# Kernel tuning notes

Measured on AMD Instinct MI355X. Metric: run time of the kernel, lower is better.

The kernel has to match this reference:

```python
import jax, jax.numpy as jnp
import numpy as np

LEAKY_ALPHA = 0.2  # TF default for tf.nn.leaky_relu

def setup_inputs() -> dict:
    key = jax.random.key(0)
    k1, k2, k3 = jax.random.split(key, 3)
    B, N, D = 8192, 2048, 128
    patient_features = jax.random.normal(k1, (B, D), dtype=jnp.float32)
    disease_nodes = jax.random.normal(k2, (N, D), dtype=jnp.float32)
    attn_kernel = jax.random.normal(k3, (2 * D, 1), dtype=jnp.float32)
    return {"patient_features": patient_features,
            "disease_nodes": disease_nodes,
            "attn_kernel": attn_kernel}

def reference(patient_features, disease_nodes, attn_kernel):
    # patient_features: [B, D]; disease_nodes: [N, D]; attn_kernel: [2D, 1]
    D = patient_features.shape[-1]
    a_p = attn_kernel[:D, 0]   # [D] acts on the patient half of the concat
    a_n = attn_kernel[D:, 0]   # [D] acts on the disease-node half
    # concat([p, n]) @ a  ==  p @ a_p  +  n @ a_n  (exact decomposition)
    scores = (patient_features @ a_p)[:, None] + (disease_nodes @ a_n)[None, :]  # [B, N]
    attn_weights = jax.nn.softmax(jax.nn.leaky_relu(scores, LEAKY_ALPHA), axis=1)  # [B, N]
    node_influence = attn_weights @ disease_nodes  # [B, D]
    return patient_features + node_influence
```

## Files before the change

kernel.cpp:

```cpp
#include <hip/hip_runtime.h>
#include <hip/hip_bf16.h>

#define LEAKY 0.2f
#define B_TOT 8192
#define N_TOT 2048
#define D_TOT 128
#define BM 16

typedef float f32x4 __attribute__((ext_vector_type(4)));
typedef short bf16x8 __attribute__((ext_vector_type(8)));
typedef unsigned short u16x8 __attribute__((ext_vector_type(8)));

static __device__ __forceinline__ unsigned short f2bf(float x) {
    return __builtin_bit_cast(unsigned short, __float2bfloat16(x));
}


__global__ __launch_bounds__(256) void prep_kernel(const float* __restrict__ disease,
                                                   const float* __restrict__ ak,
                                                   float* __restrict__ q,
                                                   uint4* __restrict__ DnTf) {
    __shared__ float tile[32][129];
    __shared__ float a_s[D_TOT];
    const int tid = threadIdx.x;
    const int b = blockIdx.x;
    const int r0 = b * 32;

    if (tid < D_TOT) a_s[tid] = ak[D_TOT + tid];
    #pragma unroll
    for (int t = 0; t < 4; ++t) {
        int idx = tid + t * 256;
        int row = idx >> 5;
        int cv = (idx & 31) * 4;
        float4 v = *(const float4*)(disease + (size_t)(r0 + row) * D_TOT + cv);
        tile[row][cv] = v.x; tile[row][cv + 1] = v.y;
        tile[row][cv + 2] = v.z; tile[row][cv + 3] = v.w;
    }
    __syncthreads();

    const int wave = tid >> 6, lane = tid & 63;
    #pragma unroll
    for (int rr = 0; rr < 8; ++rr) {
        int r = wave * 8 + rr;
        float s = tile[r][lane] * a_s[lane] + tile[r][lane + 64] * a_s[lane + 64];
        #pragma unroll
        for (int off = 32; off; off >>= 1) s += __shfl_xor(s, off);
        if (lane == 0) q[r0 + r] = s;
    }

    #pragma unroll
    for (int h = 0; h < 2; ++h) {
        const int c  = tid + h * 256;
        const int kg = c >> 7;
        const int col = c & 127;
        const int ct = col >> 4, cl = col & 15;
        unsigned u[4];
        #pragma unroll
        for (int jj = 0; jj < 4; ++jj) {
            unsigned lo = f2bf(tile[kg * 8 + 2 * jj][col]);
            unsigned hi = f2bf(tile[kg * 8 + 2 * jj + 1][col]);
            u[jj] = lo | (hi << 16);
        }
        DnTf[((size_t)b * 8 + ct) * 64 + kg * 16 + cl] = make_uint4(u[0], u[1], u[2], u[3]);
    }
}

__global__ __launch_bounds__(1024, 8) void gat_mfma(const float* __restrict__ patient,
                                                    const float* __restrict__ ak,
                                                    const float* __restrict__ q,
                                                    const unsigned short* __restrict__ DnTb,
                                                    float* __restrict__ out) {
    __shared__ __align__(16) float eq1_s[N_TOT];
    __shared__ __align__(16) float eq2_s[N_TOT];
    __shared__ float red_s[7][2][1024];
    __shared__ float a_s[D_TOT];
    __shared__ float p_s[BM], E1_s[BM], E2_s[BM], S_s[BM];
    __shared__ float red16[16];

    const int tid  = threadIdx.x;
    const int wave = tid >> 6;
    const int lane = tid & 63;
    const int b0   = blockIdx.x * BM;

    if (tid < D_TOT) a_s[tid] = ak[tid];
    __syncthreads();

    float mx = -1e30f;
    for (int i = tid; i < N_TOT; i += 1024) {
        float qq = q[i];
        eq1_s[i] = __expf(qq);
        eq2_s[i] = __expf(LEAKY * qq);
        mx = fmaxf(mx, qq);
    }
    #pragma unroll
    for (int off = 32; off; off >>= 1) mx = fmaxf(mx, __shfl_xor(mx, off));
    if (lane == 0) red16[wave] = mx;

    {
        const float* pr = patient + (size_t)(b0 + wave) * D_TOT;
        float s = pr[lane] * a_s[lane] + pr[lane + 64] * a_s[lane + 64];
        #pragma unroll
        for (int off = 32; off; off >>= 1) s += __shfl_xor(s, off);
        if (lane == 0) p_s[wave] = s;
    }
    __syncthreads();

    if (tid < BM) {
        float qmax = red16[0];
        #pragma unroll
        for (int i = 1; i < 16; ++i) qmax = fmaxf(qmax, red16[i]);
        const float pv = p_s[tid];
        const float xm = pv + qmax;
        const float m = fmaxf(xm, LEAKY * xm);
        E1_s[tid] = __expf(pv - m);
        E2_s[tid] = __expf(LEAKY * pv - m);
    }
    __syncthreads();

    {
        const float E1 = E1_s[wave], E2 = E2_s[wave];
        float s = 0.f;
        for (int n = lane; n < N_TOT; n += 64)
            s += fmaxf(E1 * eq1_s[n], E2 * eq2_s[n]);
        #pragma unroll
        for (int off = 32; off; off >>= 1) s += __shfl_xor(s, off);
        if (lane == 0) S_s[wave] = s;
    }
    __syncthreads();

    const int cl = lane & 15;
    const int kg = lane >> 4;
    const int cw = wave & 1;
    const int kq = wave >> 1;

    const float E1A = E1_s[cl], E2A = E2_s[cl];

    f32x4 acc[4] = {};

    #pragma unroll 2
    for (int kt = kq * 8; kt < kq * 8 + 8; ++kt) {
        const int gk = kt * 32 + kg * 8;
        const float4 e1a = *(const float4*)&eq1_s[gk];
        const float4 e1b = *(const float4*)&eq1_s[gk + 4];
        const float4 e2a = *(const float4*)&eq2_s[gk];
        const float4 e2b = *(const float4*)&eq2_s[gk + 4];
        bf16x8 bf[4];
        #pragma unroll
        for (int t = 0; t < 4; ++t)
            bf[t] = *(const bf16x8*)(DnTb + (((size_t)kt * 8 + cw * 4 + t) * 64 + lane) * 8);

        const float e1v[8] = {e1a.x, e1a.y, e1a.z, e1a.w, e1b.x, e1b.y, e1b.z, e1b.w};
        const float e2v[8] = {e2a.x, e2a.y, e2a.z, e2a.w, e2b.x, e2b.y, e2b.z, e2b.w};
        u16x8 aw;
        #pragma unroll
        for (int j = 0; j < 8; ++j)
            aw[j] = f2bf(fmaxf(E1A * e1v[j], E2A * e2v[j]));
        const bf16x8 a0 = __builtin_bit_cast(bf16x8, aw);

        acc[0] = __builtin_amdgcn_mfma_f32_16x16x32_bf16(a0, bf[0], acc[0], 0, 0, 0);
        acc[1] = __builtin_amdgcn_mfma_f32_16x16x32_bf16(a0, bf[1], acc[1], 0, 0, 0);
        acc[2] = __builtin_amdgcn_mfma_f32_16x16x32_bf16(a0, bf[2], acc[2], 0, 0, 0);
        acc[3] = __builtin_amdgcn_mfma_f32_16x16x32_bf16(a0, bf[3], acc[3], 0, 0, 0);
    }

    __syncthreads();
    if (kq > 0) {
        float* rb = &red_s[kq - 1][cw][0];
        #pragma unroll
        for (int t = 0; t < 4; ++t)
            #pragma unroll
            for (int i = 0; i < 4; ++i)
                rb[t * 256 + (kg * 4 + i) * 16 + cl] = acc[t][i];
    }
    __syncthreads();
    if (kq == 0) {
        #pragma unroll
        for (int t = 0; t < 4; ++t)
            #pragma unroll
            for (int i = 0; i < 4; ++i) {
                const int idx = t * 256 + (kg * 4 + i) * 16 + cl;
                float s = acc[t][i];
                #pragma unroll
                for (int j = 0; j < 7; ++j) s += red_s[j][cw][idx];
                acc[t][i] = s;
            }
        float inv[4];
        #pragma unroll
        for (int i = 0; i < 4; ++i) inv[i] = 1.0f / S_s[kg * 4 + i];
        #pragma unroll
        for (int t = 0; t < 4; ++t)
            #pragma unroll
            for (int i = 0; i < 4; ++i) {
                const int row = b0 + kg * 4 + i;
                const int col = cw * 64 + t * 16 + cl;
                out[(size_t)row * D_TOT + col] =
                    patient[(size_t)row * D_TOT + col] + acc[t][i] * inv[i];
            }
    }
}


__global__ __launch_bounds__(256) void pq_fb(const float* __restrict__ patient,
                                             const float* __restrict__ disease,
                                             const float* __restrict__ ak,
                                             float* __restrict__ p,
                                             float* __restrict__ q) {
    int gid  = blockIdx.x * blockDim.x + threadIdx.x;
    int wid  = gid >> 6;
    int lane = gid & 63;
    const float* src;
    const float* a;
    float* dst;
    if (wid < B_TOT) {
        src = patient + (size_t)wid * D_TOT; a = ak; dst = p + wid;
    } else {
        src = disease + (size_t)(wid - B_TOT) * D_TOT; a = ak + D_TOT; dst = q + (wid - B_TOT);
    }
    float s = src[lane] * a[lane] + src[lane + 64] * a[lane + 64];
    #pragma unroll
    for (int off = 32; off; off >>= 1) s += __shfl_xor(s, off);
    if (lane == 0) *dst = s;
}

#define FBP 16
#define FNT 256
__global__ __launch_bounds__(256) void gat_fb(const float* __restrict__ patient,
                                              const float* __restrict__ disease,
                                              const float* __restrict__ p,
                                              const float* __restrict__ q,
                                              float* __restrict__ out) {
    __shared__ float q_s[N_TOT];
    __shared__ float w_s[FBP][FNT];
    __shared__ float m_s[FBP], S_s[FBP], pp_s[FBP];
    const int tid = threadIdx.x;
    const int b0  = blockIdx.x * FBP;
    for (int i = tid; i < N_TOT; i += 256) q_s[i] = q[i];
    if (tid < FBP) pp_s[tid] = p[b0 + tid];
    __syncthreads();
    const int wave = tid >> 6, lane = tid & 63;
    for (int pi = wave * 4; pi < wave * 4 + 4; ++pi) {
        float pp = pp_s[pi];
        float mx = -1e30f;
        for (int n = lane; n < N_TOT; n += 64) {
            float x = pp + q_s[n]; x = x > 0.0f ? x : LEAKY * x; mx = fmaxf(mx, x);
        }
        #pragma unroll
        for (int off = 32; off; off >>= 1) mx = fmaxf(mx, __shfl_xor(mx, off));
        float sum = 0.0f;
        for (int n = lane; n < N_TOT; n += 64) {
            float x = pp + q_s[n]; x = x > 0.0f ? x : LEAKY * x; sum += __expf(x - mx);
        }
        #pragma unroll
        for (int off = 32; off; off >>= 1) sum += __shfl_xor(sum, off);
        if (lane == 0) { m_s[pi] = mx; S_s[pi] = sum; }
    }
    __syncthreads();
    const int d2 = tid & 31;
    const int pg = tid >> 5;
    const int p0 = 2 * pg, p1 = 2 * pg + 1;
    float4 acc0 = make_float4(0.f, 0.f, 0.f, 0.f);
    float4 acc1 = make_float4(0.f, 0.f, 0.f, 0.f);
    for (int n0 = 0; n0 < N_TOT; n0 += FNT) {
        __syncthreads();
        for (int i = tid; i < FBP * FNT; i += 256) {
            int pi = i >> 8;
            int nt = i & (FNT - 1);
            float x = pp_s[pi] + q_s[n0 + nt];
            x = x > 0.0f ? x : LEAKY * x;
            w_s[pi][nt] = __expf(x - m_s[pi]);
        }
        __syncthreads();
        const float* drow = disease + (size_t)n0 * D_TOT + d2 * 4;
        #pragma unroll 4
        for (int nt = 0; nt < FNT; ++nt) {
            float4 dv = *reinterpret_cast<const float4*>(drow + (size_t)nt * D_TOT);
            float w0 = w_s[p0][nt];
            float w1 = w_s[p1][nt];
            acc0.x += w0 * dv.x; acc0.y += w0 * dv.y; acc0.z += w0 * dv.z; acc0.w += w0 * dv.w;
            acc1.x += w1 * dv.x; acc1.y += w1 * dv.y; acc1.z += w1 * dv.z; acc1.w += w1 * dv.w;
        }
    }
    const float inv0 = 1.0f / S_s[p0];
    const float inv1 = 1.0f / S_s[p1];
    {
        size_t off = (size_t)(b0 + p0) * D_TOT + d2 * 4;
        float4 pf = *reinterpret_cast<const float4*>(patient + off);
        float4 o;
        o.x = pf.x + acc0.x * inv0; o.y = pf.y + acc0.y * inv0;
        o.z = pf.z + acc0.z * inv0; o.w = pf.w + acc0.w * inv0;
        *reinterpret_cast<float4*>(reinterpret_cast<float*>(out) + off) = o;
    }
    {
        size_t off = (size_t)(b0 + p1) * D_TOT + d2 * 4;
        float4 pf = *reinterpret_cast<const float4*>(patient + off);
        float4 o;
        o.x = pf.x + acc1.x * inv1; o.y = pf.y + acc1.y * inv1;
        o.z = pf.z + acc1.z * inv1; o.w = pf.w + acc1.w * inv1;
        *reinterpret_cast<float4*>(reinterpret_cast<float*>(out) + off) = o;
    }
}

extern "C" void kernel_launch(void* const* d_in, const int* in_sizes, int n_in,
                              void* d_out, int out_size, void* d_ws, size_t ws_size,
                              hipStream_t stream) {
    const float* patient = (const float*)d_in[0];
    const float* disease = (const float*)d_in[1];
    const float* ak      = (const float*)d_in[2];
    float* out = (float*)d_out;

    const size_t need_fast = (size_t)512 * 1024 + 8192;
    if (ws_size >= need_fast) {
        uint4* DnTf = (uint4*)d_ws;
        float* q    = (float*)((char*)d_ws + 512 * 1024);
        prep_kernel<<<N_TOT / 32, 256, 0, stream>>>(disease, ak, q, DnTf);
        gat_mfma<<<B_TOT / BM, 1024, 0, stream>>>(patient, ak, q,
                                                  (const unsigned short*)DnTf, out);
    } else {
        float* p = (float*)d_ws;
        float* q = p + B_TOT;
        pq_fb<<<(B_TOT + N_TOT) / 4, 256, 0, stream>>>(patient, disease, ak, p, q);
        gat_fb<<<B_TOT / FBP, 256, 0, stream>>>(patient, disease, p, q, out);
    }
}
```

Before: 29.07 us.

## Replace dense attention GEMM with sorted-threshold prefix-sum formulation

The scores are rank-1 (p_b + q_n), so the leaky-relu branch depends only on whether q_n > -p_b. The new path sorts q by rank counting and builds per-column prefix and suffix sums of exp(q)·disease and exp(0.2q)·disease. Each patient row then needs only a binary search and a few O(D) lookups instead of a full N×D product. This removes the B×N×D MFMA work but adds three small serial kernels (rank, scan, pq). It also brings fp32 cancellation risk from subtracting prefix sums, and needs a larger workspace.

New measurement: 39.78 us. +36.8%, slower.

```diff
diff --git a/kernel.cpp b/kernel.cpp
--- a/kernel.cpp
+++ b/kernel.cpp
@@ -5,7 +5,6 @@
 #define B_TOT 8192
 #define N_TOT 2048
 #define D_TOT 128
-#define BM 16
 
 typedef float f32x4 __attribute__((ext_vector_type(4)));
 typedef short bf16x8 __attribute__((ext_vector_type(8)));
@@ -14,191 +13,6 @@
 static __device__ __forceinline__ unsigned short f2bf(float x) {
     return __builtin_bit_cast(unsigned short, __float2bfloat16(x));
 }
-
-
-__global__ __launch_bounds__(256) void prep_kernel(const float* __restrict__ disease,
-                                                   const float* __restrict__ ak,
-                                                   float* __restrict__ q,
-                                                   uint4* __restrict__ DnTf) {
-    __shared__ float tile[32][129];
-    __shared__ float a_s[D_TOT];
-    const int tid = threadIdx.x;
-    const int b = blockIdx.x;
-    const int r0 = b * 32;
-
-    if (tid < D_TOT) a_s[tid] = ak[D_TOT + tid];
-    #pragma unroll
-    for (int t = 0; t < 4; ++t) {
-        int idx = tid + t * 256;
-        int row = idx >> 5;
-        int cv = (idx & 31) * 4;
-        float4 v = *(const float4*)(disease + (size_t)(r0 + row) * D_TOT + cv);
-        tile[row][cv] = v.x; tile[row][cv + 1] = v.y;
-        tile[row][cv + 2] = v.z; tile[row][cv + 3] = v.w;
-    }
-    __syncthreads();
-
-    const int wave = tid >> 6, lane = tid & 63;
-    #pragma unroll
-    for (int rr = 0; rr < 8; ++rr) {
-        int r = wave * 8 + rr;
-        float s = tile[r][lane] * a_s[lane] + tile[r][lane + 64] * a_s[lane + 64];
-        #pragma unroll
-        for (int off = 32; off; off >>= 1) s += __shfl_xor(s, off);
-        if (lane == 0) q[r0 + r] = s;
-    }
-
-    #pragma unroll
-    for (int h = 0; h < 2; ++h) {
-        const int c  = tid + h * 256;
-        const int kg = c >> 7;
-        const int col = c & 127;
-        const int ct = col >> 4, cl = col & 15;
-        unsigned u[4];
-        #pragma unroll
-        for (int jj = 0; jj < 4; ++jj) {
-            unsigned lo = f2bf(tile[kg * 8 + 2 * jj][col]);
-            unsigned hi = f2bf(tile[kg * 8 + 2 * jj + 1][col]);
-            u[jj] = lo | (hi << 16);
-        }
-        DnTf[((size_t)b * 8 + ct) * 64 + kg * 16 + cl] = make_uint4(u[0], u[1], u[2], u[3]);
-    }
-}
-
-__global__ __launch_bounds__(1024, 8) void gat_mfma(const float* __restrict__ patient,
-                                                    const float* __restrict__ ak,
-                                                    const float* __restrict__ q,
-                                                    const unsigned short* __restrict__ DnTb,
-                                                    float* __restrict__ out) {
-    __shared__ __align__(16) float eq1_s[N_TOT];
-    __shared__ __align__(16) float eq2_s[N_TOT];
-    __shared__ float red_s[7][2][1024];
-    __shared__ float a_s[D_TOT];
-    __shared__ float p_s[BM], E1_s[BM], E2_s[BM], S_s[BM];
-    __shared__ float red16[16];
-
-    const int tid  = threadIdx.x;
-    const int wave = tid >> 6;
-    const int lane = tid & 63;
-    const int b0   = blockIdx.x * BM;
-
-    if (tid < D_TOT) a_s[tid] = ak[tid];
-    __syncthreads();
-
-    float mx = -1e30f;
-    for (int i = tid; i < N_TOT; i += 1024) {
-        float qq = q[i];
-        eq1_s[i] = __expf(qq);
-        eq2_s[i] = __expf(LEAKY * qq);
-        mx = fmaxf(mx, qq);
-    }
-    #pragma unroll
-    for (int off = 32; off; off >>= 1) mx = fmaxf(mx, __shfl_xor(mx, off));
-    if (lane == 0) red16[wave] = mx;
-
-    {
-        const float* pr = patient + (size_t)(b0 + wave) * D_TOT;
-        float s = pr[lane] * a_s[lane] + pr[lane + 64] * a_s[lane + 64];
-        #pragma unroll
-        for (int off = 32; off; off >>= 1) s += __shfl_xor(s, off);
-        if (lane == 0) p_s[wave] = s;
-    }
-    __syncthreads();
-
-    if (tid < BM) {
-        float qmax = red16[0];
-        #pragma unroll
-        for (int i = 1; i < 16; ++i) qmax = fmaxf(qmax, red16[i]);
-        const float pv = p_s[tid];
-        const float xm = pv + qmax;
-        const float m = fmaxf(xm, LEAKY * xm);
-        E1_s[tid] = __expf(pv - m);
-        E2_s[tid] = __expf(LEAKY * pv - m);
-    }
-    __syncthreads();
-
-    {
-        const float E1 = E1_s[wave], E2 = E2_s[wave];
-        float s = 0.f;
-        for (int n = lane; n < N_TOT; n += 64)
-            s += fmaxf(E1 * eq1_s[n], E2 * eq2_s[n]);
-        #pragma unroll
-        for (int off = 32; off; off >>= 1) s += __shfl_xor(s, off);
-        if (lane == 0) S_s[wave] = s;
-    }
-    __syncthreads();
-
-    const int cl = lane & 15;
-    const int kg = lane >> 4;
-    const int cw = wave & 1;
-    const int kq = wave >> 1;
-
-    const float E1A = E1_s[cl], E2A = E2_s[cl];
-
-    f32x4 acc[4] = {};
-
-    #pragma unroll 2
-    for (int kt = kq * 8; kt < kq * 8 + 8; ++kt) {
-        const int gk = kt * 32 + kg * 8;
-        const float4 e1a = *(const float4*)&eq1_s[gk];
-        const float4 e1b = *(const float4*)&eq1_s[gk + 4];
-        const float4 e2a = *(const float4*)&eq2_s[gk];
-        const float4 e2b = *(const float4*)&eq2_s[gk + 4];
-        bf16x8 bf[4];
-        #pragma unroll
-        for (int t = 0; t < 4; ++t)
-            bf[t] = *(const bf16x8*)(DnTb + (((size_t)kt * 8 + cw * 4 + t) * 64 + lane) * 8);
-
-        const float e1v[8] = {e1a.x, e1a.y, e1a.z, e1a.w, e1b.x, e1b.y, e1b.z, e1b.w};
-        const float e2v[8] = {e2a.x, e2a.y, e2a.z, e2a.w, e2b.x, e2b.y, e2b.z, e2b.w};
-        u16x8 aw;
-        #pragma unroll
-        for (int j = 0; j < 8; ++j)
-            aw[j] = f2bf(fmaxf(E1A * e1v[j], E2A * e2v[j]));
-        const bf16x8 a0 = __builtin_bit_cast(bf16x8, aw);
-
-        acc[0] = __builtin_amdgcn_mfma_f32_16x16x32_bf16(a0, bf[0], acc[0], 0, 0, 0);
-        acc[1] = __builtin_amdgcn_mfma_f32_16x16x32_bf16(a0, bf[1], acc[1], 0, 0, 0);
-        acc[2] = __builtin_amdgcn_mfma_f32_16x16x32_bf16(a0, bf[2], acc[2], 0, 0, 0);
-        acc[3] = __builtin_amdgcn_mfma_f32_16x16x32_bf16(a0, bf[3], acc[3], 0, 0, 0);
-    }
-
-    __syncthreads();
-    if (kq > 0) {
-        float* rb = &red_s[kq - 1][cw][0];
-        #pragma unroll
-        for (int t = 0; t < 4; ++t)
-            #pragma unroll
-            for (int i = 0; i < 4; ++i)
-                rb[t * 256 + (kg * 4 + i) * 16 + cl] = acc[t][i];
-    }
-    __syncthreads();
-    if (kq == 0) {
-        #pragma unroll
-        for (int t = 0; t < 4; ++t)
-            #pragma unroll
-            for (int i = 0; i < 4; ++i) {
-                const int idx = t * 256 + (kg * 4 + i) * 16 + cl;
-                float s = acc[t][i];
-                #pragma unroll
-                for (int j = 0; j < 7; ++j) s += red_s[j][cw][idx];
-                acc[t][i] = s;
-            }
-        float inv[4];
-        #pragma unroll
-        for (int i = 0; i < 4; ++i) inv[i] = 1.0f / S_s[kg * 4 + i];
-        #pragma unroll
-        for (int t = 0; t < 4; ++t)
-            #pragma unroll
-            for (int i = 0; i < 4; ++i) {
-                const int row = b0 + kg * 4 + i;
-                const int col = cw * 64 + t * 16 + cl;
-                out[(size_t)row * D_TOT + col] =
-                    patient[(size_t)row * D_TOT + col] + acc[t][i] * inv[i];
-            }
-    }
-}
-
 
 __global__ __launch_bounds__(256) void pq_fb(const float* __restrict__ patient,
                                              const float* __restrict__ disease,
@@ -222,6 +36,357 @@
     if (lane == 0) *dst = s;
 }
 
+__global__ __launch_bounds__(256) void rank_kernel(const float* __restrict__ q,
+                                                   float* __restrict__ sortedq,
+                                                   float* __restrict__ eq1s,
+                                                   float* __restrict__ eq2s,
+                                                   int* __restrict__ perm) {
+    __shared__ float q_s[N_TOT];
+    const int tid = threadIdx.x;
+    for (int i = tid; i < N_TOT; i += 256) q_s[i] = q[i];
+    __syncthreads();
+    const int kl = tid >> 2, sub = tid & 3;
+    const int k = blockIdx.x * 64 + kl;
+    const float qk = q_s[k];
+    int cnt = 0;
+    const int j0 = sub * 512;
+    for (int j = j0; j < j0 + 512; ++j) {
+        float qj = q_s[j];
+        cnt += (qj < qk || (qj == qk && j < k)) ? 1 : 0;
+    }
+    cnt += __shfl_xor(cnt, 1);
+    cnt += __shfl_xor(cnt, 2);
+    if (sub == 0) {
+        sortedq[cnt] = qk;
+        perm[cnt]    = k;
+        eq1s[cnt]    = __expf(qk);
+        eq2s[cnt]    = __expf(LEAKY * qk);
+    }
+}
+
+__global__ __launch_bounds__(256) void scan_kernel(const float* __restrict__ disease,
+                                                   const float* __restrict__ eq1s,
+                                                   const float* __restrict__ eq2s,
+                                                   const int* __restrict__ perm,
+                                                   float* __restrict__ P1,
+                                                   float* __restrict__ P2,
+                                                   float* __restrict__ T1,
+                                                   float* __restrict__ T2,
+                                                   float* __restrict__ S1suf,
+                                                   float* __restrict__ S2pre) {
+    const int tid = threadIdx.x;
+    const int b = blockIdx.x;
+    if (b < 32) {
+        __shared__ int   perm_s[64];
+        __shared__ float e1l[64], e2l[64];
+        const int r0 = b * 64;
+        if (tid < 64) {
+            perm_s[tid] = perm[r0 + tid];
+            e1l[tid] = eq1s[r0 + tid];
+            e2l[tid] = eq2s[r0 + tid];
+        }
+        __syncthreads();
+        const int table = tid >> 7, col = tid & 127;
+        float run = 0.f;
+        float* Pt = table ? P2 : P1;
+        #pragma unroll 4
+        for (int j = 0; j < 64; ++j) {
+            const float d = disease[(size_t)perm_s[j] * D_TOT + col];
+            const float v = (table ? e2l[j] : e1l[j]) * d;
+            Pt[(size_t)(r0 + j) * D_TOT + col] = run;
+            run += v;
+        }
+        (table ? T2 : T1)[b * 128 + col] = run;
+    } else {
+        __shared__ float v_s[N_TOT];
+        __shared__ float wtot[4];
+        __shared__ float tot_s;
+        const int lane = tid & 63, wv = tid >> 6;
+        for (int pass = 0; pass < 2; ++pass) {
+            const float* src = pass == 0 ? eq1s : eq2s;
+            for (int i = tid; i < N_TOT; i += 256) v_s[i] = src[i];
+            __syncthreads();
+            float s[8];
+            float run = 0.f;
+            #pragma unroll
+            for (int i = 0; i < 8; ++i) { run += v_s[tid * 8 + i]; s[i] = run; }
+            float incl = run;
+            #pragma unroll
+            for (int off = 1; off < 64; off <<= 1) {
+                float v = __shfl_up(incl, off);
+                if (lane >= off) incl += v;
+            }
+            if (lane == 63) wtot[wv] = incl;
+            __syncthreads();
+            float woff = 0.f;
+            for (int w = 0; w < wv; ++w) woff += wtot[w];
+            const float base = woff + incl - run;
+            if (tid == 255) tot_s = woff + incl;
+            __syncthreads();
+            const float tot = tot_s;
+            if (pass == 0) {
+                #pragma unroll
+                for (int i = 0; i < 8; ++i) {
+                    float EP = base + (i ? s[i - 1] : 0.f);
+                    S1suf[tid * 8 + i] = tot - EP;
+                }
+                if (tid == 255) S1suf[N_TOT] = 0.f;
+            } else {
+                #pragma unroll
+                for (int i = 0; i < 8; ++i)
+                    S2pre[tid * 8 + i] = base + (i ? s[i - 1] : 0.f);
+                if (tid == 255) S2pre[N_TOT] = tot;
+            }
+            __syncthreads();
+        }
+    }
+}
+
+__global__ __launch_bounds__(256) void gat_ps(const float* __restrict__ patient,
+                                              const float* __restrict__ p,
+                                              const float* __restrict__ sortedq,
+                                              const float* __restrict__ P1,
+                                              const float* __restrict__ P2,
+                                              const float* __restrict__ T1,
+                                              const float* __restrict__ T2,
+                                              const float* __restrict__ S1suf,
+                                              const float* __restrict__ S2pre,
+                                              float* __restrict__ out) {
+    __shared__ float sq[N_TOT];
+    __shared__ float suf1[33][128];
+    __shared__ float pre2[33][128];
+    __shared__ float e1_s[32], e2_s[32], inv_s[32];
+    __shared__ int   c_s[32];
+    const int tid = threadIdx.x;
+    const int b0 = blockIdx.x * 32;
+
+    for (int i = tid; i < N_TOT; i += 256) sq[i] = sortedq[i];
+
+    if (tid < 128) {
+        float r = 0.f;
+        suf1[32][tid] = 0.f;
+        for (int b = 31; b >= 0; --b) { r += T1[b * 128 + tid]; suf1[b][tid] = r; }
+    } else {
+        const int col = tid - 128;
+        float r = 0.f;
+        for (int b = 0; b < 32; ++b) { pre2[b][col] = r; r += T2[b * 128 + col]; }
+        pre2[32][col] = r;
+    }
+    __syncthreads();
+
+    if (tid < 32) {
+        const float pv = p[b0 + tid];
+        const float qmax = sq[N_TOT - 1];
+        const float xm = pv + qmax;
+        const float m = fmaxf(xm, LEAKY * xm);
+        const float E1 = __expf(pv - m);
+        const float E2 = __expf(LEAKY * pv - m);
+        const float thr = -pv;
+        int lo = 0, hi = N_TOT;
+        while (lo < hi) {
+            int mid = (lo + hi) >> 1;
+            if (sq[mid] <= thr) lo = mid + 1; else hi = mid;
+        }
+        const float S = E1 * S1suf[lo] + E2 * S2pre[lo];
+        e1_s[tid] = E1; e2_s[tid] = E2; inv_s[tid] = 1.0f / S; c_s[tid] = lo;
+    }
+    __syncthreads();
+
+    const int row = tid >> 3;
+    const int cb = (tid & 7) * 16;
+    const int gr = b0 + row;
+    const int c = c_s[row];
+    const int bc = c >> 6;
+    const float E1 = e1_s[row], E2 = e2_s[row], inv = inv_s[row];
+    const bool has = (c < N_TOT);
+
+    #pragma unroll
+    for (int i = 0; i < 4; ++i) {
+        const int col = cb + i * 4;
+        float4 p1 = make_float4(0.f, 0.f, 0.f, 0.f);
+        float4 p2 = make_float4(0.f, 0.f, 0.f, 0.f);
+        if (has) {
+            p1 = *(const float4*)&P1[(size_t)c * D_TOT + col];
+            p2 = *(const float4*)&P2[(size_t)c * D_TOT + col];
+        }
+        const float4 pat = *(const float4*)&patient[(size_t)gr * D_TOT + col];
+        float4 o;
+        o.x = pat.x + (E1 * (suf1[bc][col + 0] - p1.x) + E2 * (pre2[bc][col + 0] + p2.x)) * inv;
+        o.y = pat.y + (E1 * (suf1[bc][col + 1] - p1.y) + E2 * (pre2[bc][col + 1] + p2.y)) * inv;
+        o.z = pat.z + (E1 * (suf1[bc][col + 2] - p1.z) + E2 * (pre2[bc][col + 2] + p2.z)) * inv;
+        o.w = pat.w + (E1 * (suf1[bc][col + 3] - p1.w) + E2 * (pre2[bc][col + 3] + p2.w)) * inv;
+        *(float4*)&out[(size_t)gr * D_TOT + col] = o;
+    }
+}
+
+#define MBM 16
+__global__ __launch_bounds__(256) void prep_kernel(const float* __restrict__ disease,
+                                                   const float* __restrict__ ak,
+                                                   float* __restrict__ q,
+                                                   uint4* __restrict__ DnTf) {
+    __shared__ float tile[32][129];
+    __shared__ float a_s[D_TOT];
+    const int tid = threadIdx.x;
+    const int b = blockIdx.x;
+    const int r0 = b * 32;
+    if (tid < D_TOT) a_s[tid] = ak[D_TOT + tid];
+    #pragma unroll
+    for (int t = 0; t < 4; ++t) {
+        int idx = tid + t * 256;
+        int row = idx >> 5;
+        int cv = (idx & 31) * 4;
+        float4 v = *(const float4*)(disease + (size_t)(r0 + row) * D_TOT + cv);
+        tile[row][cv] = v.x; tile[row][cv + 1] = v.y;
+        tile[row][cv + 2] = v.z; tile[row][cv + 3] = v.w;
+    }
+    __syncthreads();
+    const int wave = tid >> 6, lane = tid & 63;
+    #pragma unroll
+    for (int rr = 0; rr < 8; ++rr) {
+        int r = wave * 8 + rr;
+        float s = tile[r][lane] * a_s[lane] + tile[r][lane + 64] * a_s[lane + 64];
+        #pragma unroll
+        for (int off = 32; off; off >>= 1) s += __shfl_xor(s, off);
+        if (lane == 0) q[r0 + r] = s;
+    }
+    #pragma unroll
+    for (int h = 0; h < 2; ++h) {
+        const int c  = tid + h * 256;
+        const int kg = c >> 7;
+        const int col = c & 127;
+        const int ct = col >> 4, cl = col & 15;
+        unsigned u[4];
+        #pragma unroll
+        for (int jj = 0; jj < 4; ++jj) {
+            unsigned lo = f2bf(tile[kg * 8 + 2 * jj][col]);
+            unsigned hi = f2bf(tile[kg * 8 + 2 * jj + 1][col]);
+            u[jj] = lo | (hi << 16);
+        }
+        DnTf[((size_t)b * 8 + ct) * 64 + kg * 16 + cl] = make_uint4(u[0], u[1], u[2], u[3]);
+    }
+}
+
+__global__ __launch_bounds__(1024, 8) void gat_mfma(const float* __restrict__ patient,
+                                                    const float* __restrict__ ak,
+                                                    const float* __restrict__ q,
+                                                    const unsigned short* __restrict__ DnTb,
+                                                    float* __restrict__ out) {
+    __shared__ __align__(16) float eq1_s[N_TOT];
+    __shared__ __align__(16) float eq2_s[N_TOT];
+    __shared__ float red_s[7][2][1024];
+    __shared__ float a_s[D_TOT];
+    __shared__ float p_s[MBM], E1_s[MBM], E2_s[MBM], S_s[MBM];
+    __shared__ float red16[16];
+    const int tid  = threadIdx.x;
+    const int wave = tid >> 6;
+    const int lane = tid & 63;
+    const int b0   = blockIdx.x * MBM;
+    if (tid < D_TOT) a_s[tid] = ak[tid];
+    __syncthreads();
+    float mx = -1e30f;
+    for (int i = tid; i < N_TOT; i += 1024) {
+        float qq = q[i];
+        eq1_s[i] = __expf(qq);
+        eq2_s[i] = __expf(LEAKY * qq);
+        mx = fmaxf(mx, qq);
+    }
+    #pragma unroll
+    for (int off = 32; off; off >>= 1) mx = fmaxf(mx, __shfl_xor(mx, off));
+    if (lane == 0) red16[wave] = mx;
+    {
+        const float* pr = patient + (size_t)(b0 + wave) * D_TOT;
+        float s = pr[lane] * a_s[lane] + pr[lane + 64] * a_s[lane + 64];
+        #pragma unroll
+        for (int off = 32; off; off >>= 1) s += __shfl_xor(s, off);
+        if (lane == 0) p_s[wave] = s;
+    }
+    __syncthreads();
+    if (tid < MBM) {
+        float qmax = red16[0];
+        #pragma unroll
+        for (int i = 1; i < 16; ++i) qmax = fmaxf(qmax, red16[i]);
+        const float pv = p_s[tid];
+        const float xm = pv + qmax;
+        const float m = fmaxf(xm, LEAKY * xm);
+        E1_s[tid] = __expf(pv - m);
+        E2_s[tid] = __expf(LEAKY * pv - m);
+    }
+    __syncthreads();
+    {
+        const float E1 = E1_s[wave], E2 = E2_s[wave];
+        float s = 0.f;
+        for (int n = lane; n < N_TOT; n += 64)
+            s += fmaxf(E1 * eq1_s[n], E2 * eq2_s[n]);
+        #pragma unroll
+        for (int off = 32; off; off >>= 1) s += __shfl_xor(s, off);
+        if (lane == 0) S_s[wave] = s;
+    }
+    __syncthreads();
+    const int cl = lane & 15;
+    const int kg = lane >> 4;
+    const int cw = wave & 1;
+    const int kq = wave >> 1;
+    const float E1A = E1_s[cl], E2A = E2_s[cl];
+    f32x4 acc[4] = {};
+    #pragma unroll 2
+    for (int kt = kq * 8; kt < kq * 8 + 8; ++kt) {
+        const int gk = kt * 32 + kg * 8;
+        const float4 e1a = *(const float4*)&eq1_s[gk];
+        const float4 e1b = *(const float4*)&eq1_s[gk + 4];
+        const float4 e2a = *(const float4*)&eq2_s[gk];
+        const float4 e2b = *(const float4*)&eq2_s[gk + 4];
+        bf16x8 bf[4];
+        #pragma unroll
+        for (int t = 0; t < 4; ++t)
+            bf[t] = *(const bf16x8*)(DnTb + (((size_t)kt * 8 + cw * 4 + t) * 64 + lane) * 8);
+        const float e1v[8] = {e1a.x, e1a.y, e1a.z, e1a.w, e1b.x, e1b.y, e1b.z, e1b.w};
+        const float e2v[8] = {e2a.x, e2a.y, e2a.z, e2a.w, e2b.x, e2b.y, e2b.z, e2b.w};
+        u16x8 aw;
+        #pragma unroll
+        for (int j = 0; j < 8; ++j)
+            aw[j] = f2bf(fmaxf(E1A * e1v[j], E2A * e2v[j]));
+        const bf16x8 a0 = __builtin_bit_cast(bf16x8, aw);
+        acc[0] = __builtin_amdgcn_mfma_f32_16x16x32_bf16(a0, bf[0], acc[0], 0, 0, 0);
+        acc[1] = __builtin_amdgcn_mfma_f32_16x16x32_bf16(a0, bf[1], acc[1], 0, 0, 0);
+        acc[2] = __builtin_amdgcn_mfma_f32_16x16x32_bf16(a0, bf[2], acc[2], 0, 0, 0);
+        acc[3] = __builtin_amdgcn_mfma_f32_16x16x32_bf16(a0, bf[3], acc[3], 0, 0, 0);
+    }
+    __syncthreads();
+    if (kq > 0) {
+        float* rb = &red_s[kq - 1][cw][0];
+        #pragma unroll
+        for (int t = 0; t < 4; ++t)
+            #pragma unroll
+            for (int i = 0; i < 4; ++i)
+                rb[t * 256 + (kg * 4 + i) * 16 + cl] = acc[t][i];
+    }
+    __syncthreads();
+    if (kq == 0) {
+        #pragma unroll
+        for (int t = 0; t < 4; ++t)
+            #pragma unroll
+            for (int i = 0; i < 4; ++i) {
+                const int idx = t * 256 + (kg * 4 + i) * 16 + cl;
+                float s = acc[t][i];
+                #pragma unroll
+                for (int j = 0; j < 7; ++j) s += red_s[j][cw][idx];
+                acc[t][i] = s;
+            }
+        float inv[4];
+        #pragma unroll
+        for (int i = 0; i < 4; ++i) inv[i] = 1.0f / S_s[kg * 4 + i];
+        #pragma unroll
+        for (int t = 0; t < 4; ++t)
+            #pragma unroll
+            for (int i = 0; i < 4; ++i) {
+                const int row = b0 + kg * 4 + i;
+                const int col = cw * 64 + t * 16 + cl;
+                out[(size_t)row * D_TOT + col] =
+                    patient[(size_t)row * D_TOT + col] + acc[t][i] * inv[i];
+            }
+    }
+}
+
 #define FBP 16
 #define FNT 256
 __global__ __launch_bounds__(256) void gat_fb(const float* __restrict__ patient,
@@ -307,14 +472,46 @@
     const float* disease = (const float*)d_in[1];
     const float* ak      = (const float*)d_in[2];
     float* out = (float*)d_out;
-
-    const size_t need_fast = (size_t)512 * 1024 + 8192;
+    char* w = (char*)d_ws;
+
+    const size_t oP1 = 0;
+    const size_t oP2 = 1048576;
+    const size_t oT1 = 2097152;
+    const size_t oT2 = 2113536;
+    const size_t oS1 = 2129920;
+    const size_t oS2 = 2138368;
+    const size_t oSQ = 2146816;
+    const size_t oE1 = 2155008;
+    const size_t oE2 = 2163200;
+    const size_t oPM = 2171392;
+    const size_t oQ  = 2179584;
+    const size_t oP  = 2187776;
+    const size_t need_fast = 2220544;
+    const size_t need_mid  = (size_t)512 * 1024 + 8192;
+
     if (ws_size >= need_fast) {
+        float* P1 = (float*)(w + oP1);
+        float* P2 = (float*)(w + oP2);
+        float* T1 = (float*)(w + oT1);
+        float* T2 = (float*)(w + oT2);
+        float* S1 = (float*)(w + oS1);
+        float* S2 = (float*)(w + oS2);
+        float* sq = (float*)(w + oSQ);
+        float* e1 = (float*)(w + oE1);
+        float* e2 = (float*)(w + oE2);
+        int*   pm = (int*)  (w + oPM);
+        float* q  = (float*)(w + oQ);
+        float* p  = (float*)(w + oP);
+        pq_fb<<<(B_TOT + N_TOT) / 4, 256, 0, stream>>>(patient, disease, ak, p, q);
+        rank_kernel<<<32, 256, 0, stream>>>(q, sq, e1, e2, pm);
+        scan_kernel<<<33, 256, 0, stream>>>(disease, e1, e2, pm, P1, P2, T1, T2, S1, S2);
+        gat_ps<<<B_TOT / 32, 256, 0, stream>>>(patient, p, sq, P1, P2, T1, T2, S1, S2, out);
+    } else if (ws_size >= need_mid) {
         uint4* DnTf = (uint4*)d_ws;
-        float* q    = (float*)((char*)d_ws + 512 * 1024);
+        float* q    = (float*)(w + 512 * 1024);
         prep_kernel<<<N_TOT / 32, 256, 0, stream>>>(disease, ak, q, DnTf);
-        gat_mfma<<<B_TOT / BM, 1024, 0, stream>>>(patient, ak, q,
-                                                  (const unsigned short*)DnTf, out);
+        gat_mfma<<<B_TOT / MBM, 1024, 0, stream>>>(patient, ak, q,
+                                                   (const unsigned short*)DnTf, out);
     } else {
         float* p = (float*)d_ws;
         float* q = p + B_TOT;
```
